# Kernel optimization log

Measured on AMD Instinct MI355X. Metric: run time of the kernel, lower is better.

## Reference

```python
import jax, jax.numpy as jnp
import numpy as np

EPS = 1e-5

def layer_norm(x, g, b):
    m = jnp.mean(x, axis=-1, keepdims=True)
    v = jnp.var(x, axis=-1, keepdims=True)
    return (x - m) / jnp.sqrt(v + EPS) * g + b

def setup_inputs() -> dict:
    key = jax.random.key(0)
    B, N, D, H, F = 2, 2048, 1024, 16, 4096
    ks = jax.random.split(key, 12)
    s = 0.02
    return {
        "x": jax.random.normal(ks[0], (B, N, D), dtype=jnp.float32),
        "wq": jax.random.normal(ks[1], (D, D), dtype=jnp.float32) * s,
        "bq": jnp.zeros((D,), jnp.float32),
        "wk": jax.random.normal(ks[2], (D, D), dtype=jnp.float32) * s,
        "bk": jnp.zeros((D,), jnp.float32),
        "wv": jax.random.normal(ks[3], (D, D), dtype=jnp.float32) * s,
        "bv": jnp.zeros((D,), jnp.float32),
        "g1": jnp.ones((D,), jnp.float32),
        "b1": jnp.zeros((D,), jnp.float32),
        "g2": jnp.ones((D,), jnp.float32),
        "b2": jnp.zeros((D,), jnp.float32),
        "w1": jax.random.normal(ks[4], (D, F), dtype=jnp.float32) * s,
        "bw1": jnp.zeros((F,), jnp.float32),
        "gf": jnp.ones((F,), jnp.float32),
        "bf": jnp.zeros((F,), jnp.float32),
        "w2": jax.random.normal(ks[5], (F, D), dtype=jnp.float32) * s,
        "bw2": jnp.zeros((D,), jnp.float32),
        "num_heads": 16,
    }

def reference(x, wq, bq, wk, bk, wv, bv, g1, b1, g2, b2, w1, bw1, gf, bf, w2, bw2, num_heads):
    B, N, D = x.shape
    H = num_heads
    E = D // H
    h = layer_norm(x, g1, b1)
    q = (h @ wq + bq).reshape(B, N, H, E).transpose(0, 2, 1, 3)  # B H N E
    k = (h @ wk + bk).reshape(B, N, H, E).transpose(0, 2, 1, 3)
    v = (h @ wv + bv).reshape(B, N, H, E).transpose(0, 2, 1, 3)
    # NOTE: original scales by 1/sqrt(1/emb_dim) == sqrt(emb_dim)
    scale = jnp.sqrt(jnp.float32(D))
    score = jnp.einsum('bhne,bhme->bhnm', q, k) * scale  # B H N N
    w = jax.nn.softmax(score, axis=-1)
    attn = jnp.einsum('bhnm,bhme->bhne', w, v)
    attn = attn.transpose(0, 2, 1, 3).reshape(B, N, D)
    x = x + attn  # dropout = identity in eval
    h2 = layer_norm(x, g2, b2)
    # MLP: Linear -> (Dropout) -> LayerNorm -> ReLU -> Linear; NO residual add (faithful to source)
    u = layer_norm(h2 @ w1 + bw1, gf, bf)
    return jax.nn.relu(u) @ w2 + bw2
```

## Files before the change

kernel.cpp:

```cpp
#include <hip/hip_runtime.h>

typedef unsigned short u16;
typedef _Float16 f16;
typedef _Float16 f16x8 __attribute__((ext_vector_type(8)));
typedef float f32x4 __attribute__((ext_vector_type(4)));
typedef unsigned short u16x4 __attribute__((ext_vector_type(4)));
typedef unsigned int u32x4 __attribute__((ext_vector_type(4)));

__device__ __forceinline__ u16 f2h(float f) {
    f16 h = (f16)f;
    return *reinterpret_cast<u16*>(&h);
}
__device__ __forceinline__ float h2f(u16 u) {
    f16 h = *reinterpret_cast<f16*>(&u);
    return (float)h;
}

__device__ __forceinline__ float exp2v(float x) { return __builtin_amdgcn_exp2f(x); }

__device__ __forceinline__ unsigned cvtpkh(float lo, float hi) {
    unsigned r;
    asm("v_cvt_pkrtz_f16_f32 %0, %1, %2" : "=v"(r) : "v"(lo), "v"(hi));
    return r;
}

__device__ __forceinline__ void gload16(const u16* g, u16* l) {
    __builtin_amdgcn_global_load_lds((const __attribute__((address_space(1))) unsigned int*)g,
                                     (__attribute__((address_space(3))) unsigned int*)l, 16, 0, 0);
}

#define RAW_BARRIER() __builtin_amdgcn_s_barrier()
#define WAITCNT_VM(N) asm volatile("s_waitcnt vmcnt(" #N ")" ::: "memory")

__device__ __forceinline__ int xcd_swz(int bid, int nwg) {
    return (bid & 7) * (nwg >> 3) + (bid >> 3);
}

__global__ void transpose_cast3(const float* __restrict__ W0, u16* __restrict__ T0,
                                const float* __restrict__ W1, u16* __restrict__ T1,
                                const float* __restrict__ W2, u16* __restrict__ T2,
                                int K, int N) {
    __shared__ float t[32][33];
    const float* W = (blockIdx.z == 0) ? W0 : (blockIdx.z == 1) ? W1 : W2;
    u16* Wt = (blockIdx.z == 0) ? T0 : (blockIdx.z == 1) ? T1 : T2;
    const int n0 = blockIdx.x * 32, k0 = blockIdx.y * 32;
    const int tx = threadIdx.x, ty = threadIdx.y;
#pragma unroll
    for (int i = 0; i < 32; i += 8)
        t[ty + i][tx] = W[(size_t)(k0 + ty + i) * N + n0 + tx];
    __syncthreads();
#pragma unroll
    for (int i = 0; i < 32; i += 8)
        Wt[(size_t)(n0 + ty + i) * K + k0 + tx] = f2h(t[tx][ty + i]);
}

__global__ void transpose_cast(const float* __restrict__ W, u16* __restrict__ Wt,
                               int K, int N) {
    __shared__ float t[32][33];
    const int n0 = blockIdx.x * 32, k0 = blockIdx.y * 32;
    const int tx = threadIdx.x, ty = threadIdx.y;
#pragma unroll
    for (int i = 0; i < 32; i += 8)
        t[ty + i][tx] = W[(size_t)(k0 + ty + i) * N + n0 + tx];
    __syncthreads();
#pragma unroll
    for (int i = 0; i < 32; i += 8)
        Wt[(size_t)(n0 + ty + i) * K + k0 + tx] = f2h(t[tx][ty + i]);
}

__global__ __launch_bounds__(256) void ln_f32_f16(const float* __restrict__ in,
                                                  const float* __restrict__ g,
                                                  const float* __restrict__ b,
                                                  u16* __restrict__ out) {
    constexpr int Dl = 1024;
    const int row = blockIdx.x, tid = threadIdx.x;
    const float4 v = *(const float4*)&in[(size_t)row * Dl + tid * 4];
    const float* vp = (const float*)&v;
    float s = v.x + v.y + v.z + v.w;
    float s2 = v.x * v.x + v.y * v.y + v.z * v.z + v.w * v.w;
#pragma unroll
    for (int off = 32; off; off >>= 1) { s += __shfl_xor(s, off); s2 += __shfl_xor(s2, off); }
    __shared__ float red[8];
    const int lane = tid & 63, wid = tid >> 6;
    if (lane == 0) { red[wid] = s; red[4 + wid] = s2; }
    __syncthreads();
    s = red[0] + red[1] + red[2] + red[3];
    s2 = red[4] + red[5] + red[6] + red[7];
    const float mean = s * (1.0f / Dl);
    const float rstd = rsqrtf(s2 * (1.0f / Dl) - mean * mean + 1e-5f);
    u16x4 pk;
#pragma unroll
    for (int i = 0; i < 4; ++i) {
        const int col = tid * 4 + i;
        pk[i] = f2h((vp[i] - mean) * rstd * g[col] + b[col]);
    }
    *(u16x4*)&out[(size_t)row * Dl + tid * 4] = pk;
}

__global__ __launch_bounds__(256) void ln_relu_f16(u16* __restrict__ mid,
                                                   const float* __restrict__ g,
                                                   const float* __restrict__ b) {
    constexpr int Fl = 4096;
    const int row = blockIdx.x, tid = threadIdx.x;
    u16* rp = mid + (size_t)row * Fl;
    float v[16];
    u32x4 raw[2];
#pragma unroll
    for (int c = 0; c < 2; ++c) raw[c] = *(const u32x4*)&rp[tid * 16 + c * 8];
#pragma unroll
    for (int c = 0; c < 2; ++c)
#pragma unroll
        for (int j = 0; j < 4; ++j) {
            const unsigned u = raw[c][j];
            v[c * 8 + j * 2] = h2f((u16)(u & 0xffffu));
            v[c * 8 + j * 2 + 1] = h2f((u16)(u >> 16));
        }
    float s = 0.f, s2 = 0.f;
#pragma unroll
    for (int i = 0; i < 16; ++i) { s += v[i]; s2 += v[i] * v[i]; }
#pragma unroll
    for (int off = 32; off; off >>= 1) { s += __shfl_xor(s, off); s2 += __shfl_xor(s2, off); }
    __shared__ float red[8];
    const int lane = tid & 63, wid = tid >> 6;
    if (lane == 0) { red[wid] = s; red[4 + wid] = s2; }
    __syncthreads();
    s = red[0] + red[1] + red[2] + red[3];
    s2 = red[4] + red[5] + red[6] + red[7];
    const float mean = s * (1.0f / Fl);
    const float rstd = rsqrtf(s2 * (1.0f / Fl) - mean * mean + 1e-5f);
    unsigned w[8];
#pragma unroll
    for (int j = 0; j < 8; ++j) {
        const int col = tid * 16 + j * 2;
        const float y0 = fmaxf((v[j * 2] - mean) * rstd * g[col] + b[col], 0.f);
        const float y1 = fmaxf((v[j * 2 + 1] - mean) * rstd * g[col + 1] + b[col + 1], 0.f);
        w[j] = (unsigned)f2h(y0) | ((unsigned)f2h(y1) << 16);
    }
    *(u32x4*)&rp[tid * 16] = *(u32x4*)&w[0];
    *(u32x4*)&rp[tid * 16 + 8] = *(u32x4*)&w[4];
}

template <int EPI, int BN>
__global__ __launch_bounds__(256, 4) void gemm_f16(const u16* __restrict__ A,
                                                   const u16* __restrict__ Bt,
                                                   const float* __restrict__ bias,
                                                   u16* __restrict__ outB,
                                                   float* __restrict__ outF,
                                                   int M_, int N_, int K_) {
    constexpr int BK = 32;
    constexpr int NJ = BN / 32;
    __shared__ u16 As[2][128 * BK];
    __shared__ u16 Bs[2][BN * BK];
    const int tid = threadIdx.x;
    const int lane = tid & 63;
    const int wid = tid >> 6;
    const int swz = xcd_swz(blockIdx.y * gridDim.x + blockIdx.x, gridDim.x * gridDim.y);
    const int m0 = (swz / gridDim.x) * 128;
    const int n0 = (swz % gridDim.x) * BN;
    const int wr = (wid >> 1) * 64;
    const int wc = (wid & 1) * (BN / 2);
    const int fr = lane & 15;
    const int fg = 8 * ((lane >> 4) ^ ((fr >> 1) & 3));

    const int srow = wid * 32 + (lane >> 2);
    const int srB = wid * (BN / 4) + (lane >> 2);
    const int scol = 8 * ((lane & 3) ^ ((lane >> 3) & 3));
    const u16* pa0 = A + (size_t)(m0 + srow) * K_ + scol;
    const u16* pa1 = pa0 + (size_t)16 * K_;
    const u16* pb0 = Bt + (size_t)(n0 + srB) * K_ + scol;
    const u16* pb1 = pb0 + (size_t)16 * K_;
    const int aoff = wid * 1024;
    const int boff = wid * (BN / 4) * BK;

    auto stage = [&](int k0, int buf) {
        gload16(pa0 + k0, &As[buf][aoff]);
        gload16(pa1 + k0, &As[buf][aoff + 512]);
        gload16(pb0 + k0, &Bs[buf][boff]);
        if constexpr (BN == 128) gload16(pb1 + k0, &Bs[buf][boff + 512]);
    };

    f32x4 acc[4][NJ] = {};
    const int nt = K_ / BK;

    stage(0, 0);
    WAITCNT_VM(0);
    RAW_BARRIER();

    for (int t = 0; t < nt; ++t) {
        const int buf = t & 1;
        if (t + 1 < nt) stage((t + 1) * BK, buf ^ 1);
        f16x8 aF[4], bF[NJ];
#pragma unroll
        for (int i = 0; i < 4; ++i) aF[i] = *(const f16x8*)&As[buf][(wr + i * 16 + fr) * BK + fg];
#pragma unroll
        for (int j = 0; j < NJ; ++j) bF[j] = *(const f16x8*)&Bs[buf][(wc + j * 16 + fr) * BK + fg];
#pragma unroll
        for (int i = 0; i < 4; ++i)
#pragma unroll
            for (int j = 0; j < NJ; ++j)
                acc[i][j] = __builtin_amdgcn_mfma_f32_16x16x32_f16(aF[i], bF[j], acc[i][j], 0, 0, 0);
        WAITCNT_VM(0);
        RAW_BARRIER();
    }

    const int g4 = (lane >> 4) * 4;
#pragma unroll
    for (int i = 0; i < 4; ++i) {
#pragma unroll
        for (int j = 0; j < NJ; ++j) {
            const int mb = m0 + wr + i * 16 + g4;
            const int nb = n0 + wc + j * 16 + fr;
            const float bv = bias[nb];
            if constexpr (EPI == 0) {
#pragma unroll
                for (int r = 0; r < 4; ++r)
                    outB[(size_t)(mb + r) * N_ + nb] = f2h(acc[i][j][r] + bv);
            } else {
#pragma unroll
                for (int r = 0; r < 4; ++r)
                    outF[(size_t)(mb + r) * N_ + nb] = acc[i][j][r] + bv;
            }
        }
    }
}

__global__ __launch_bounds__(256, 4) void gemm_f16_splitk(const u16* __restrict__ A,
                                                          const u16* __restrict__ Bt,
                                                          float* __restrict__ p0,
                                                          float* __restrict__ p1,
                                                          int M_, int N_, int K_) {
    constexpr int BK = 32, BN = 64;
    __shared__ u16 As[2][128 * BK];
    __shared__ u16 Bs[2][BN * BK];
    const int tid = threadIdx.x;
    const int lane = tid & 63;
    const int wid = tid >> 6;
    const int swz = xcd_swz(blockIdx.y * gridDim.x + blockIdx.x, gridDim.x * gridDim.y);
    const int m0 = (swz / gridDim.x) * 128;
    const int n0 = (swz % gridDim.x) * BN;
    const int kBase = blockIdx.z * (K_ >> 1);
    float* dst = blockIdx.z ? p1 : p0;
    const int wr = (wid >> 1) * 64;
    const int wc = (wid & 1) * (BN / 2);
    const int fr = lane & 15;
    const int fg = 8 * ((lane >> 4) ^ ((fr >> 1) & 3));

    const int srow = wid * 32 + (lane >> 2);
    const int srB = wid * (BN / 4) + (lane >> 2);
    const int scol = 8 * ((lane & 3) ^ ((lane >> 3) & 3));
    const u16* pa0 = A + (size_t)(m0 + srow) * K_ + kBase + scol;
    const u16* pa1 = pa0 + (size_t)16 * K_;
    const u16* pb0 = Bt + (size_t)(n0 + srB) * K_ + kBase + scol;
    const int aoff = wid * 1024;
    const int boff = wid * (BN / 4) * BK;

    auto stage = [&](int k0, int buf) {
        gload16(pa0 + k0, &As[buf][aoff]);
        gload16(pa1 + k0, &As[buf][aoff + 512]);
        gload16(pb0 + k0, &Bs[buf][boff]);
    };

    f32x4 acc[4][2] = {};
    const int nt = (K_ >> 1) / BK;

    stage(0, 0);
    WAITCNT_VM(0);
    RAW_BARRIER();

    for (int t = 0; t < nt; ++t) {
        const int buf = t & 1;
        if (t + 1 < nt) stage((t + 1) * BK, buf ^ 1);
        f16x8 aF[4], bF[2];
#pragma unroll
        for (int i = 0; i < 4; ++i) aF[i] = *(const f16x8*)&As[buf][(wr + i * 16 + fr) * BK + fg];
#pragma unroll
        for (int j = 0; j < 2; ++j) bF[j] = *(const f16x8*)&Bs[buf][(wc + j * 16 + fr) * BK + fg];
#pragma unroll
        for (int i = 0; i < 4; ++i)
#pragma unroll
            for (int j = 0; j < 2; ++j)
                acc[i][j] = __builtin_amdgcn_mfma_f32_16x16x32_f16(aF[i], bF[j], acc[i][j], 0, 0, 0);
        WAITCNT_VM(0);
        RAW_BARRIER();
    }

    const int g4 = (lane >> 4) * 4;
#pragma unroll
    for (int i = 0; i < 4; ++i)
#pragma unroll
        for (int j = 0; j < 2; ++j) {
            const int mb = m0 + wr + i * 16 + g4;
            const int nb = n0 + wc + j * 16 + fr;
#pragma unroll
            for (int r = 0; r < 4; ++r)
                dst[(size_t)(mb + r) * N_ + nb] = acc[i][j][r];
        }
}

__global__ __launch_bounds__(256) void reduce2_bias(const float* __restrict__ p0,
                                                    const float* __restrict__ p1,
                                                    const float* __restrict__ bias,
                                                    float* __restrict__ out, int N_) {
    const size_t i4 = (size_t)blockIdx.x * 256 + threadIdx.x;
    const float4 a = ((const float4*)p0)[i4];
    const float4 b = ((const float4*)p1)[i4];
    const int col4 = (int)(i4 % (N_ / 4));
    const float4 bi = ((const float4*)bias)[col4];
    float4 o;
    o.x = a.x + b.x + bi.x;
    o.y = a.y + b.y + bi.y;
    o.z = a.z + b.z + bi.z;
    o.w = a.w + b.w + bi.w;
    ((float4*)out)[i4] = o;
}

__global__ __launch_bounds__(256, 4) void gemm_qkv(const u16* __restrict__ A,
                                                   const u16* __restrict__ qW,
                                                   const u16* __restrict__ kW,
                                                   const u16* __restrict__ vW,
                                                   const float* __restrict__ bq,
                                                   const float* __restrict__ bk,
                                                   const float* __restrict__ bv,
                                                   u16* __restrict__ qb, u16* __restrict__ kb,
                                                   u16* __restrict__ vtb,
                                                   int M_, int K_) {
    constexpr int BK = 32;
    __shared__ u16 As[2][128 * BK];
    __shared__ u16 Bs[2][64 * BK];
    const int tid = threadIdx.x;
    const int lane = tid & 63;
    const int wid = tid >> 6;
    const int swz = xcd_swz(blockIdx.y * gridDim.x + blockIdx.x, gridDim.x * gridDim.y);
    const int bx = swz % gridDim.x;
    const int region = bx >> 4;
    const int n0 = (bx & 15) * 64;
    const int m0 = (swz / gridDim.x) * 128;
    const int wr = (wid >> 1) * 64;
    const int wc = (wid & 1) * 32;
    const int fr = lane & 15;
    const int fg = 8 * ((lane >> 4) ^ ((fr >> 1) & 3));

    const int srow = wid * 32 + (lane >> 2);
    const int srB = wid * 16 + (lane >> 2);
    const int scol = 8 * ((lane & 3) ^ ((lane >> 3) & 3));

    const u16* B = (region == 0) ? qW : (region == 1) ? kW : vW;
    const u16* pa0 = A + (size_t)(m0 + srow) * K_ + scol;
    const u16* pa1 = pa0 + (size_t)16 * K_;
    const u16* pb = B + (size_t)(n0 + srB) * K_ + scol;
    const int aoff = wid * 1024;
    const int boff = wid * 512;

    auto stage = [&](int k0, int buf) {
        gload16(pa0 + k0, &As[buf][aoff]);
        gload16(pa1 + k0, &As[buf][aoff + 512]);
        gload16(pb + k0, &Bs[buf][boff]);
    };

    f32x4 acc[4][2] = {};
    const int nt = K_ / BK;

    stage(0, 0);
    WAITCNT_VM(0);
    RAW_BARRIER();

    for (int t = 0; t < nt; ++t) {
        const int buf = t & 1;
        if (t + 1 < nt) stage((t + 1) * BK, buf ^ 1);
        f16x8 aF[4], bF[2];
#pragma unroll
        for (int i = 0; i < 4; ++i) aF[i] = *(const f16x8*)&As[buf][(wr + i * 16 + fr) * BK + fg];
#pragma unroll
        for (int j = 0; j < 2; ++j) bF[j] = *(const f16x8*)&Bs[buf][(wc + j * 16 + fr) * BK + fg];
#pragma unroll
        for (int i = 0; i < 4; ++i)
#pragma unroll
            for (int j = 0; j < 2; ++j)
                acc[i][j] = __builtin_amdgcn_mfma_f32_16x16x32_f16(aF[i], bF[j], acc[i][j], 0, 0, 0);
        WAITCNT_VM(0);
        RAW_BARRIER();
    }

    const float* bias = (region == 0) ? bq : (region == 1) ? bk : bv;
    const float scale = (region == 0) ? 32.f : 1.f;
    const int g4 = (lane >> 4) * 4;
#pragma unroll
    for (int i = 0; i < 4; ++i) {
#pragma unroll
        for (int j = 0; j < 2; ++j) {
            const int mb = m0 + wr + i * 16 + g4;
            const int nb = n0 + wc + j * 16 + fr;
            const float bv_ = bias[nb];
            const int h = nb >> 6, e = nb & 63;
            if (region < 2) {
                u16* outp = (region == 0) ? qb : kb;
#pragma unroll
                for (int r = 0; r < 4; ++r) {
                    const int m = mb + r;
                    const size_t idx = ((size_t)((m >> 11) * 16 + h) * 2048 + (m & 2047)) * 64 + e;
                    outp[idx] = f2h((acc[i][j][r] + bv_) * scale);
                }
            } else {
                const int b_ = mb >> 11, np = mb & 2047;
                u16x4 pk;
#pragma unroll
                for (int r = 0; r < 4; ++r) pk[r] = f2h(acc[i][j][r] + bv_);
                *(u16x4*)&vtb[((size_t)(b_ * 16 + h) * 64 + e) * 2048 + np] = pk;
            }
        }
    }
}

__global__ __launch_bounds__(512, 4) void attn_kernel(const u16* __restrict__ q,
                                                      const u16* __restrict__ k,
                                                      const u16* __restrict__ vt,
                                                      const float* __restrict__ x,
                                                      float* __restrict__ x2) {
    constexpr int N = 2048, E = 64, KB = 64, NT = N / KB;
    constexpr float L2E = 1.4426950408889634f;
    __shared__ u16 Ks[2][64 * 64];
    __shared__ u16 Vs[2][64 * 64];
    __shared__ unsigned Ps[8][16][36];

    const int tid = threadIdx.x;
    const int lane = tid & 63;
    const int wid = tid >> 6;
    const int swzb = xcd_swz(blockIdx.x, gridDim.x);
    const int bh = swzb >> 4;
    const int q0 = (swzb & 15) * 128;
    const u16* qh = q + (size_t)bh * N * E;
    const u16* kh = k + (size_t)bh * N * E;
    const u16* vh = vt + (size_t)bh * E * N;

    const int fr = lane & 15;
    const int fgrp = lane >> 4;
    const int fg8 = fgrp * 8;
    int pc[2];
#pragma unroll
    for (int ks = 0; ks < 2; ++ks) pc[ks] = 8 * (((ks << 2) + fgrp) ^ (fr & 7));

    const int srow = wid * 8 + (lane >> 3);
    const int swc = 8 * ((lane & 7) ^ (lane >> 3));
    u16* dK = &Ks[0][wid * 8 * 64];
    u16* dV = &Vs[0][wid * 8 * 64];
    constexpr int BUFO = 64 * 64;

    f16x8 qf[2];
#pragma unroll
    for (int ks = 0; ks < 2; ++ks)
        qf[ks] = *(const f16x8*)&qh[(size_t)(q0 + wid * 16 + fr) * E + ks * 32 + fg8];

    auto stage = [&](int t, int buf) {
        const size_t kb = (size_t)t * KB;
        gload16(kh + (kb + srow) * E + swc, dK + buf * BUFO);
        gload16(vh + (size_t)srow * N + kb + swc, dV + buf * BUFO);
    };

    f32x4 o[4] = {};
    float mrow = -1e30f, lpart = 0.f;

    stage(0, 0);

    for (int t = 0; t < NT; ++t) {
        const int buf = t & 1;
        RAW_BARRIER();
        if (t + 1 < NT) {
            stage(t + 1, buf ^ 1);
            WAITCNT_VM(2);
        } else {
            WAITCNT_VM(0);
        }
        RAW_BARRIER();

        const u16* KK = &Ks[buf][0];
        const u16* VV = &Vs[buf][0];

        f32x4 s[4] = {};
        __builtin_amdgcn_s_setprio(1);
#pragma unroll
        for (int fn = 0; fn < 4; ++fn)
#pragma unroll
            for (int ks = 0; ks < 2; ++ks) {
                const f16x8 kf = *(const f16x8*)&KK[(fn * 16 + fr) * 64 + pc[ks]];
                s[fn] = __builtin_amdgcn_mfma_f32_16x16x32_f16(kf, qf[ks], s[fn], 0, 0, 0);
            }
        __builtin_amdgcn_s_setprio(0);

        float lmax = fmaxf(fmaxf(fmaxf(s[0][0], s[0][1]), fmaxf(s[0][2], s[0][3])),
                           fmaxf(fmaxf(s[1][0], s[1][1]), fmaxf(s[1][2], s[1][3])));
        lmax = fmaxf(lmax, fmaxf(fmaxf(fmaxf(s[2][0], s[2][1]), fmaxf(s[2][2], s[2][3])),
                                 fmaxf(fmaxf(s[3][0], s[3][1]), fmaxf(s[3][2], s[3][3]))));
        if (!__all(lmax <= mrow + 8.f)) {
            float m2 = fmaxf(lmax, __shfl_xor(lmax, 16));
            m2 = fmaxf(m2, __shfl_xor(m2, 32));
            const float mnew = fmaxf(mrow, m2);
            const float fac = exp2v((mrow - mnew) * L2E);
            mrow = mnew;
            lpart *= fac;
            float fo[4];
#pragma unroll
            for (int r = 0; r < 4; ++r) fo[r] = __shfl(fac, fgrp * 4 + r);
#pragma unroll
            for (int fe = 0; fe < 4; ++fe)
#pragma unroll
                for (int r = 0; r < 4; ++r) o[fe][r] *= fo[r];
        }

        const float nml = -mrow * L2E;
#pragma unroll
        for (int fn = 0; fn < 4; ++fn) {
            const float p0 = exp2v(fmaf(s[fn][0], L2E, nml));
            const float p1 = exp2v(fmaf(s[fn][1], L2E, nml));
            const float p2 = exp2v(fmaf(s[fn][2], L2E, nml));
            const float p3 = exp2v(fmaf(s[fn][3], L2E, nml));
            lpart += (p0 + p1) + (p2 + p3);
            uint2 w;
            w.x = cvtpkh(p0, p1);
            w.y = cvtpkh(p2, p3);
            *(uint2*)&Ps[wid][fr][fn * 8 + fgrp * 2] = w;
        }

        const u16* prow = (const u16*)&Ps[wid][fr][0];
        f16x8 pf[2];
#pragma unroll
        for (int ks = 0; ks < 2; ++ks) pf[ks] = *(const f16x8*)&prow[ks * 32 + fg8];
        __builtin_amdgcn_s_setprio(1);
#pragma unroll
        for (int fe = 0; fe < 4; ++fe)
#pragma unroll
            for (int ks = 0; ks < 2; ++ks) {
                const f16x8 vf = *(const f16x8*)&VV[(fe * 16 + fr) * 64 + pc[ks]];
                o[fe] = __builtin_amdgcn_mfma_f32_16x16x32_f16(pf[ks], vf, o[fe], 0, 0, 0);
            }
        __builtin_amdgcn_s_setprio(0);
    }

    float lsum = lpart + __shfl_xor(lpart, 16);
    lsum += __shfl_xor(lsum, 32);
    float rl[4];
#pragma unroll
    for (int r = 0; r < 4; ++r) rl[r] = 1.0f / __shfl(lsum, fgrp * 4 + r);

    const int b_ = bh >> 4, h_ = bh & 15;
#pragma unroll
    for (int fe = 0; fe < 4; ++fe)
#pragma unroll
        for (int r = 0; r < 4; ++r) {
            const int npos = q0 + wid * 16 + fgrp * 4 + r;
            const size_t idx = ((size_t)(b_ * 2048 + npos)) * 1024 + h_ * 64 + fe * 16 + fr;
            x2[idx] = x[idx] + o[fe][r] * rl[r];
        }
}

extern "C" void kernel_launch(void* const* d_in, const int* in_sizes, int n_in,
                              void* d_out, int out_size, void* d_ws, size_t ws_size,
                              hipStream_t stream) {
    const float* x = (const float*)d_in[0];
    const float* wq = (const float*)d_in[1];
    const float* bq = (const float*)d_in[2];
    const float* wk = (const float*)d_in[3];
    const float* bk = (const float*)d_in[4];
    const float* wv = (const float*)d_in[5];
    const float* bv = (const float*)d_in[6];
    const float* g1 = (const float*)d_in[7];
    const float* b1 = (const float*)d_in[8];
    const float* g2 = (const float*)d_in[9];
    const float* b2 = (const float*)d_in[10];
    const float* w1 = (const float*)d_in[11];
    const float* bw1 = (const float*)d_in[12];
    const float* gf = (const float*)d_in[13];
    const float* bf = (const float*)d_in[14];
    const float* w2 = (const float*)d_in[15];
    const float* bw2 = (const float*)d_in[16];
    float* out = (float*)d_out;

    constexpr int Bc = 2, Nc = 2048, Dc = 1024, Fc = 4096, Mc = 4096;

    char* ws = (char*)d_ws;
    auto alloc = [&](size_t bytes) {
        char* p = ws;
        ws += (bytes + 255) & ~(size_t)255;
        return p;
    };
    u16* wqt = (u16*)alloc((size_t)Dc * Dc * 2);
    u16* wkt = (u16*)alloc((size_t)Dc * Dc * 2);
    u16* wvt = (u16*)alloc((size_t)Dc * Dc * 2);
    u16* w1t = (u16*)alloc((size_t)Dc * Fc * 2);
    u16* w2t = (u16*)alloc((size_t)Fc * Dc * 2);
    char* region = (char*)alloc((size_t)Mc * Dc * 2 * 4);
    u16* h1 = (u16*)region;
    u16* qb = h1 + (size_t)Mc * Dc;
    u16* kb = qb + (size_t)Mc * Dc;
    u16* vtb = kb + (size_t)Mc * Dc;
    u16* mid = (u16*)region;
    float* x2 = (float*)alloc((size_t)Mc * Dc * 4);
    u16* h2 = (u16*)alloc((size_t)Mc * Dc * 2);
    float* p1 = (float*)alloc((size_t)Mc * Dc * 4);
    float* p0 = x2;

    const dim3 tb(32, 8);
    transpose_cast3<<<dim3(Dc / 32, Dc / 32, 3), tb, 0, stream>>>(wq, wqt, wk, wkt, wv, wvt, Dc, Dc);
    transpose_cast<<<dim3(Fc / 32, Dc / 32), tb, 0, stream>>>(w1, w1t, Dc, Fc);
    transpose_cast<<<dim3(Dc / 32, Fc / 32), tb, 0, stream>>>(w2, w2t, Fc, Dc);

    ln_f32_f16<<<Mc, 256, 0, stream>>>(x, g1, b1, h1);

    gemm_qkv<<<dim3(48, Mc / 128), 256, 0, stream>>>(h1, wqt, wkt, wvt, bq, bk, bv,
                                                     qb, kb, vtb, Mc, Dc);

    attn_kernel<<<Bc * 16 * (Nc / 128), 512, 0, stream>>>(qb, kb, vtb, x, x2);

    ln_f32_f16<<<Mc, 256, 0, stream>>>(x2, g2, b2, h2);

    gemm_f16<0, 128><<<dim3(Fc / 128, Mc / 128), 256, 0, stream>>>(h2, w1t, bw1, mid, nullptr, Mc, Fc, Dc);

    ln_relu_f16<<<Mc, 256, 0, stream>>>(mid, gf, bf);

    gemm_f16_splitk<<<dim3(Dc / 64, Mc / 128, 2), 256, 0, stream>>>(mid, w2t, p0, p1, Mc, Dc, Fc);
    reduce2_bias<<<(Mc * Dc) / 1024, 256, 0, stream>>>(p0, p1, bw2, out, Dc);
}
```

Measured before the change: 260.5 us.

## Split attention KV range in two and merge partials in combine kernel

Each attention block now handles only half of the key/value sequence, doubling the grid from 512 to 1024 blocks so more CUs are busy at once. Partial outputs are stored in fp16 with per-row max and sum, and a new combine kernel merges them with log-sum-exp weights and adds the residual. The cost is an extra launch, extra global traffic for the partial results, and fp16 rounding of the partial outputs. The launch-bounds occupancy hint also drops from 4 to 3.

```diff
diff --git a/kernel.cpp b/kernel.cpp
--- a/kernel.cpp
+++ b/kernel.cpp
@@ -411,12 +411,13 @@
     }
 }
 
-__global__ __launch_bounds__(512, 4) void attn_kernel(const u16* __restrict__ q,
+__global__ __launch_bounds__(512, 3) void attn_kernel(const u16* __restrict__ q,
                                                       const u16* __restrict__ k,
                                                       const u16* __restrict__ vt,
-                                                      const float* __restrict__ x,
-                                                      float* __restrict__ x2) {
-    constexpr int N = 2048, E = 64, KB = 64, NT = N / KB;
+                                                      u16* __restrict__ op,
+                                                      float* __restrict__ mA,
+                                                      float* __restrict__ lA) {
+    constexpr int N = 2048, E = 64, KB = 64, NT = 16;
     constexpr float L2E = 1.4426950408889634f;
     __shared__ u16 Ks[2][64 * 64];
     __shared__ u16 Vs[2][64 * 64];
@@ -426,8 +427,10 @@
     const int lane = tid & 63;
     const int wid = tid >> 6;
     const int swzb = xcd_swz(blockIdx.x, gridDim.x);
-    const int bh = swzb >> 4;
     const int q0 = (swzb & 15) * 128;
+    const int half = (swzb >> 4) & 1;
+    const int bh = swzb >> 5;
+    const int kv0 = half * 1024;
     const u16* qh = q + (size_t)bh * N * E;
     const u16* kh = k + (size_t)bh * N * E;
     const u16* vh = vt + (size_t)bh * E * N;
@@ -451,7 +454,7 @@
         qf[ks] = *(const f16x8*)&qh[(size_t)(q0 + wid * 16 + fr) * E + ks * 32 + fg8];
 
     auto stage = [&](int t, int buf) {
-        const size_t kb = (size_t)t * KB;
+        const size_t kb = (size_t)kv0 + (size_t)t * KB;
         gload16(kh + (kb + srow) * E + swc, dK + buf * BUFO);
         gload16(vh + (size_t)srow * N + kb + swc, dV + buf * BUFO);
     };
@@ -537,19 +540,55 @@
 
     float lsum = lpart + __shfl_xor(lpart, 16);
     lsum += __shfl_xor(lsum, 32);
+
+    const int rowg = (half * 32 + bh) * 2048 + q0 + wid * 16;
+    if (fgrp == 0) {
+        mA[rowg + fr] = mrow;
+        lA[rowg + fr] = lsum;
+    }
+
     float rl[4];
 #pragma unroll
     for (int r = 0; r < 4; ++r) rl[r] = 1.0f / __shfl(lsum, fgrp * 4 + r);
 
+#pragma unroll
+    for (int fe = 0; fe < 4; ++fe)
+#pragma unroll
+        for (int r = 0; r < 4; ++r)
+            op[((size_t)rowg + fgrp * 4 + r) * 64 + fe * 16 + fr] = f2h(o[fe][r] * rl[r]);
+}
+
+__global__ __launch_bounds__(256) void attn_combine(const u16* __restrict__ op,
+                                                    const float* __restrict__ mA,
+                                                    const float* __restrict__ lA,
+                                                    const float* __restrict__ x,
+                                                    float* __restrict__ x2) {
+    constexpr float L2E = 1.4426950408889634f;
+    const int gid = blockIdx.x * 256 + threadIdx.x;
+    const int row = gid >> 4;
+    const int e0 = (gid & 15) * 4;
+    const float m0 = mA[row], m1 = mA[65536 + row];
+    const float l0 = lA[row], l1 = lA[65536 + row];
+    const float m = fmaxf(m0, m1);
+    const float w0 = l0 * exp2v((m0 - m) * L2E);
+    const float w1 = l1 * exp2v((m1 - m) * L2E);
+    const float inv = 1.0f / (w0 + w1);
+    const float c0 = w0 * inv, c1 = w1 * inv;
+
+    const size_t oi = (size_t)row * 64 + e0;
+    const uint2 r0 = *(const uint2*)&op[oi];
+    const uint2 r1 = *(const uint2*)&op[(size_t)65536 * 64 + oi];
+
+    const int bh = row >> 11, n = row & 2047;
     const int b_ = bh >> 4, h_ = bh & 15;
-#pragma unroll
-    for (int fe = 0; fe < 4; ++fe)
-#pragma unroll
-        for (int r = 0; r < 4; ++r) {
-            const int npos = q0 + wid * 16 + fgrp * 4 + r;
-            const size_t idx = ((size_t)(b_ * 2048 + npos)) * 1024 + h_ * 64 + fe * 16 + fr;
-            x2[idx] = x[idx] + o[fe][r] * rl[r];
-        }
+    const size_t xi = ((size_t)(b_ * 2048 + n)) * 1024 + h_ * 64 + e0;
+    const float4 xv = *(const float4*)&x[xi];
+    float4 ov;
+    ov.x = xv.x + c0 * h2f((u16)(r0.x & 0xffffu)) + c1 * h2f((u16)(r1.x & 0xffffu));
+    ov.y = xv.y + c0 * h2f((u16)(r0.x >> 16)) + c1 * h2f((u16)(r1.x >> 16));
+    ov.z = xv.z + c0 * h2f((u16)(r0.y & 0xffffu)) + c1 * h2f((u16)(r1.y & 0xffffu));
+    ov.w = xv.w + c0 * h2f((u16)(r0.y >> 16)) + c1 * h2f((u16)(r1.y >> 16));
+    *(float4*)&x2[xi] = ov;
 }
 
 extern "C" void kernel_launch(void* const* d_in, const int* in_sizes, int n_in,
@@ -597,6 +636,9 @@
     u16* h2 = (u16*)alloc((size_t)Mc * Dc * 2);
     float* p1 = (float*)alloc((size_t)Mc * Dc * 4);
     float* p0 = x2;
+    u16* op = (u16*)p1;
+    float* mArr = (float*)alloc((size_t)2 * 32 * 2048 * 4);
+    float* lArr = (float*)alloc((size_t)2 * 32 * 2048 * 4);
 
     const dim3 tb(32, 8);
     transpose_cast3<<<dim3(Dc / 32, Dc / 32, 3), tb, 0, stream>>>(wq, wqt, wk, wkt, wv, wvt, Dc, Dc);
@@ -608,7 +650,8 @@
     gemm_qkv<<<dim3(48, Mc / 128), 256, 0, stream>>>(h1, wqt, wkt, wvt, bq, bk, bv,
                                                      qb, kb, vtb, Mc, Dc);
 
-    attn_kernel<<<Bc * 16 * (Nc / 128), 512, 0, stream>>>(qb, kb, vtb, x, x2);
+    attn_kernel<<<Bc * 16 * (Nc / 128) * 2, 512, 0, stream>>>(qb, kb, vtb, op, mArr, lArr);
+    attn_combine<<<(32 * Nc * 16) / 256, 256, 0, stream>>>(op, mArr, lArr, x, x2);
 
     ln_f32_f16<<<Mc, 256, 0, stream>>>(x2, g2, b2, h2);
 
```

Result: slower. 270.8 us (+3.9%).

## Process two query sub-tiles per wave in attention to reuse K/V fragments

Applied to the files above, without the earlier changes.

The attention block shrinks from 8 to 4 waves, and each wave now handles 32 query rows as two 16-row sub-tiles instead of one. Each K and V fragment read from LDS feeds two MFMAs, halving LDS reads per unit of compute, and each wave issues twice as many staging loads. The cost is roughly double the accumulator and score registers, reflected in the change of launch bounds to (256,2), which may lower occupancy and latency hiding.

```diff
diff --git a/kernel.cpp b/kernel.cpp
--- a/kernel.cpp
+++ b/kernel.cpp
@@ -411,7 +411,7 @@
     }
 }
 
-__global__ __launch_bounds__(512, 4) void attn_kernel(const u16* __restrict__ q,
+__global__ __launch_bounds__(256, 2) void attn_kernel(const u16* __restrict__ q,
                                                       const u16* __restrict__ k,
                                                       const u16* __restrict__ vt,
                                                       const float* __restrict__ x,
@@ -420,7 +420,7 @@
     constexpr float L2E = 1.4426950408889634f;
     __shared__ u16 Ks[2][64 * 64];
     __shared__ u16 Vs[2][64 * 64];
-    __shared__ unsigned Ps[8][16][36];
+    __shared__ unsigned Ps[4][32][36];
 
     const int tid = threadIdx.x;
     const int lane = tid & 63;
@@ -439,25 +439,29 @@
 #pragma unroll
     for (int ks = 0; ks < 2; ++ks) pc[ks] = 8 * (((ks << 2) + fgrp) ^ (fr & 7));
 
-    const int srow = wid * 8 + (lane >> 3);
+    const int srow = wid * 16 + (lane >> 3);
     const int swc = 8 * ((lane & 7) ^ (lane >> 3));
-    u16* dK = &Ks[0][wid * 8 * 64];
-    u16* dV = &Vs[0][wid * 8 * 64];
+    u16* dK = &Ks[0][wid * 16 * 64];
+    u16* dV = &Vs[0][wid * 16 * 64];
     constexpr int BUFO = 64 * 64;
 
-    f16x8 qf[2];
-#pragma unroll
-    for (int ks = 0; ks < 2; ++ks)
-        qf[ks] = *(const f16x8*)&qh[(size_t)(q0 + wid * 16 + fr) * E + ks * 32 + fg8];
+    f16x8 qf[2][2];
+#pragma unroll
+    for (int qs = 0; qs < 2; ++qs)
+#pragma unroll
+        for (int ks = 0; ks < 2; ++ks)
+            qf[qs][ks] = *(const f16x8*)&qh[(size_t)(q0 + wid * 32 + qs * 16 + fr) * E + ks * 32 + fg8];
 
     auto stage = [&](int t, int buf) {
         const size_t kb = (size_t)t * KB;
         gload16(kh + (kb + srow) * E + swc, dK + buf * BUFO);
+        gload16(kh + (kb + srow + 8) * E + swc, dK + buf * BUFO + 8 * 64);
         gload16(vh + (size_t)srow * N + kb + swc, dV + buf * BUFO);
+        gload16(vh + (size_t)(srow + 8) * N + kb + swc, dV + buf * BUFO + 8 * 64);
     };
 
-    f32x4 o[4] = {};
-    float mrow = -1e30f, lpart = 0.f;
+    f32x4 o[2][4] = {};
+    float mrow[2] = {-1e30f, -1e30f}, lpart[2] = {0.f, 0.f};
 
     stage(0, 0);
 
@@ -466,7 +470,7 @@
         RAW_BARRIER();
         if (t + 1 < NT) {
             stage(t + 1, buf ^ 1);
-            WAITCNT_VM(2);
+            WAITCNT_VM(4);
         } else {
             WAITCNT_VM(0);
         }
@@ -475,81 +479,99 @@
         const u16* KK = &Ks[buf][0];
         const u16* VV = &Vs[buf][0];
 
-        f32x4 s[4] = {};
+        f32x4 s[2][4] = {};
         __builtin_amdgcn_s_setprio(1);
 #pragma unroll
         for (int fn = 0; fn < 4; ++fn)
 #pragma unroll
             for (int ks = 0; ks < 2; ++ks) {
                 const f16x8 kf = *(const f16x8*)&KK[(fn * 16 + fr) * 64 + pc[ks]];
-                s[fn] = __builtin_amdgcn_mfma_f32_16x16x32_f16(kf, qf[ks], s[fn], 0, 0, 0);
+                s[0][fn] = __builtin_amdgcn_mfma_f32_16x16x32_f16(kf, qf[0][ks], s[0][fn], 0, 0, 0);
+                s[1][fn] = __builtin_amdgcn_mfma_f32_16x16x32_f16(kf, qf[1][ks], s[1][fn], 0, 0, 0);
             }
         __builtin_amdgcn_s_setprio(0);
 
-        float lmax = fmaxf(fmaxf(fmaxf(s[0][0], s[0][1]), fmaxf(s[0][2], s[0][3])),
-                           fmaxf(fmaxf(s[1][0], s[1][1]), fmaxf(s[1][2], s[1][3])));
-        lmax = fmaxf(lmax, fmaxf(fmaxf(fmaxf(s[2][0], s[2][1]), fmaxf(s[2][2], s[2][3])),
-                                 fmaxf(fmaxf(s[3][0], s[3][1]), fmaxf(s[3][2], s[3][3]))));
-        if (!__all(lmax <= mrow + 8.f)) {
-            float m2 = fmaxf(lmax, __shfl_xor(lmax, 16));
-            m2 = fmaxf(m2, __shfl_xor(m2, 32));
-            const float mnew = fmaxf(mrow, m2);
-            const float fac = exp2v((mrow - mnew) * L2E);
-            mrow = mnew;
-            lpart *= fac;
-            float fo[4];
-#pragma unroll
-            for (int r = 0; r < 4; ++r) fo[r] = __shfl(fac, fgrp * 4 + r);
-#pragma unroll
-            for (int fe = 0; fe < 4; ++fe)
-#pragma unroll
-                for (int r = 0; r < 4; ++r) o[fe][r] *= fo[r];
-        }
-
-        const float nml = -mrow * L2E;
-#pragma unroll
-        for (int fn = 0; fn < 4; ++fn) {
-            const float p0 = exp2v(fmaf(s[fn][0], L2E, nml));
-            const float p1 = exp2v(fmaf(s[fn][1], L2E, nml));
-            const float p2 = exp2v(fmaf(s[fn][2], L2E, nml));
-            const float p3 = exp2v(fmaf(s[fn][3], L2E, nml));
-            lpart += (p0 + p1) + (p2 + p3);
-            uint2 w;
-            w.x = cvtpkh(p0, p1);
-            w.y = cvtpkh(p2, p3);
-            *(uint2*)&Ps[wid][fr][fn * 8 + fgrp * 2] = w;
-        }
-
-        const u16* prow = (const u16*)&Ps[wid][fr][0];
-        f16x8 pf[2];
-#pragma unroll
-        for (int ks = 0; ks < 2; ++ks) pf[ks] = *(const f16x8*)&prow[ks * 32 + fg8];
+        float lmax[2];
+#pragma unroll
+        for (int qs = 0; qs < 2; ++qs) {
+            float a = fmaxf(fmaxf(s[qs][0][0], s[qs][0][1]), fmaxf(s[qs][0][2], s[qs][0][3]));
+            float b = fmaxf(fmaxf(s[qs][1][0], s[qs][1][1]), fmaxf(s[qs][1][2], s[qs][1][3]));
+            float c = fmaxf(fmaxf(s[qs][2][0], s[qs][2][1]), fmaxf(s[qs][2][2], s[qs][2][3]));
+            float d = fmaxf(fmaxf(s[qs][3][0], s[qs][3][1]), fmaxf(s[qs][3][2], s[qs][3][3]));
+            lmax[qs] = fmaxf(fmaxf(a, b), fmaxf(c, d));
+        }
+        if (!__all(lmax[0] <= mrow[0] + 8.f && lmax[1] <= mrow[1] + 8.f)) {
+#pragma unroll
+            for (int qs = 0; qs < 2; ++qs) {
+                float m2 = fmaxf(lmax[qs], __shfl_xor(lmax[qs], 16));
+                m2 = fmaxf(m2, __shfl_xor(m2, 32));
+                const float mnew = fmaxf(mrow[qs], m2);
+                const float fac = exp2v((mrow[qs] - mnew) * L2E);
+                mrow[qs] = mnew;
+                lpart[qs] *= fac;
+                float fo[4];
+#pragma unroll
+                for (int r = 0; r < 4; ++r) fo[r] = __shfl(fac, fgrp * 4 + r);
+#pragma unroll
+                for (int fe = 0; fe < 4; ++fe)
+#pragma unroll
+                    for (int r = 0; r < 4; ++r) o[qs][fe][r] *= fo[r];
+            }
+        }
+
+#pragma unroll
+        for (int qs = 0; qs < 2; ++qs) {
+            const float nml = -mrow[qs] * L2E;
+#pragma unroll
+            for (int fn = 0; fn < 4; ++fn) {
+                const float p0 = exp2v(fmaf(s[qs][fn][0], L2E, nml));
+                const float p1 = exp2v(fmaf(s[qs][fn][1], L2E, nml));
+                const float p2 = exp2v(fmaf(s[qs][fn][2], L2E, nml));
+                const float p3 = exp2v(fmaf(s[qs][fn][3], L2E, nml));
+                lpart[qs] += (p0 + p1) + (p2 + p3);
+                uint2 w;
+                w.x = cvtpkh(p0, p1);
+                w.y = cvtpkh(p2, p3);
+                *(uint2*)&Ps[wid][qs * 16 + fr][fn * 8 + fgrp * 2] = w;
+            }
+        }
+
+        f16x8 pf[2][2];
+#pragma unroll
+        for (int qs = 0; qs < 2; ++qs) {
+            const u16* prow = (const u16*)&Ps[wid][qs * 16 + fr][0];
+#pragma unroll
+            for (int ks = 0; ks < 2; ++ks) pf[qs][ks] = *(const f16x8*)&prow[ks * 32 + fg8];
+        }
         __builtin_amdgcn_s_setprio(1);
 #pragma unroll
         for (int fe = 0; fe < 4; ++fe)
 #pragma unroll
             for (int ks = 0; ks < 2; ++ks) {
                 const f16x8 vf = *(const f16x8*)&VV[(fe * 16 + fr) * 64 + pc[ks]];
-                o[fe] = __builtin_amdgcn_mfma_f32_16x16x32_f16(pf[ks], vf, o[fe], 0, 0, 0);
+                o[0][fe] = __builtin_amdgcn_mfma_f32_16x16x32_f16(pf[0][ks], vf, o[0][fe], 0, 0, 0);
+                o[1][fe] = __builtin_amdgcn_mfma_f32_16x16x32_f16(pf[1][ks], vf, o[1][fe], 0, 0, 0);
             }
         __builtin_amdgcn_s_setprio(0);
     }
 
-    float lsum = lpart + __shfl_xor(lpart, 16);
-    lsum += __shfl_xor(lsum, 32);
-    float rl[4];
-#pragma unroll
-    for (int r = 0; r < 4; ++r) rl[r] = 1.0f / __shfl(lsum, fgrp * 4 + r);
-
     const int b_ = bh >> 4, h_ = bh & 15;
 #pragma unroll
-    for (int fe = 0; fe < 4; ++fe)
-#pragma unroll
-        for (int r = 0; r < 4; ++r) {
-            const int npos = q0 + wid * 16 + fgrp * 4 + r;
-            const size_t idx = ((size_t)(b_ * 2048 + npos)) * 1024 + h_ * 64 + fe * 16 + fr;
-            x2[idx] = x[idx] + o[fe][r] * rl[r];
-        }
+    for (int qs = 0; qs < 2; ++qs) {
+        float lsum = lpart[qs] + __shfl_xor(lpart[qs], 16);
+        lsum += __shfl_xor(lsum, 32);
+        float rl[4];
+#pragma unroll
+        for (int r = 0; r < 4; ++r) rl[r] = 1.0f / __shfl(lsum, fgrp * 4 + r);
+#pragma unroll
+        for (int fe = 0; fe < 4; ++fe)
+#pragma unroll
+            for (int r = 0; r < 4; ++r) {
+                const int npos = q0 + wid * 32 + qs * 16 + fgrp * 4 + r;
+                const size_t idx = ((size_t)(b_ * 2048 + npos)) * 1024 + h_ * 64 + fe * 16 + fr;
+                x2[idx] = x[idx] + o[qs][fe][r] * rl[r];
+            }
+    }
 }
 
 extern "C" void kernel_launch(void* const* d_in, const int* in_sizes, int n_in,
@@ -608,7 +630,7 @@
     gemm_qkv<<<dim3(48, Mc / 128), 256, 0, stream>>>(h1, wqt, wkt, wvt, bq, bk, bv,
                                                      qb, kb, vtb, Mc, Dc);
 
-    attn_kernel<<<Bc * 16 * (Nc / 128), 512, 0, stream>>>(qb, kb, vtb, x, x2);
+    attn_kernel<<<Bc * 16 * (Nc / 128), 256, 0, stream>>>(qb, kb, vtb, x, x2);
 
     ln_f32_f16<<<Mc, 256, 0, stream>>>(x2, g2, b2, h2);
 
```

After: 264.9 us. About the same (+1.7%).
